# Kernel tuning notes

Measured on AMD Instinct MI355X. Metric: run time of the kernel, lower is better.

The kernel has to match this reference:

```python
import jax, jax.numpy as jnp
import numpy as np

B = 16
NUM_CN = 25000
NUM_VN = 50000
NUM_EDGES = 200000
D_EMBED = 16
D_HIDDEN = 32
D_MSG = 16


def setup_inputs() -> dict:
    key = jax.random.key(0)
    ks = jax.random.split(key, 16)
    def w(k, fan_in, fan_out):
        return jax.random.normal(k, (fan_in, fan_out), dtype=jnp.float32) / jnp.sqrt(jnp.float32(fan_in))
    return {
        "h_from_x": jax.random.normal(ks[0], (B, NUM_CN, D_EMBED), dtype=jnp.float32),
        "h_from_z": jax.random.normal(ks[1], (B, NUM_CN, D_EMBED), dtype=jnp.float32),
        "h_to": jax.random.normal(ks[2], (B, NUM_VN, D_EMBED), dtype=jnp.float32),
        "syndrome_x": jax.random.randint(ks[3], (B, NUM_CN), 0, 2, dtype=jnp.int32),
        "syndrome_z": jax.random.randint(ks[4], (B, NUM_CN), 0, 2, dtype=jnp.int32),
        "from_ind_x": jax.random.randint(ks[5], (NUM_EDGES,), 0, NUM_CN, dtype=jnp.int32),
        "to_ind_x": jax.random.randint(ks[6], (NUM_EDGES,), 0, NUM_VN, dtype=jnp.int32),
        "from_ind_z": jax.random.randint(ks[7], (NUM_EDGES,), 0, NUM_CN, dtype=jnp.int32),
        "to_ind_z": jax.random.randint(ks[8], (NUM_EDGES,), 0, NUM_VN, dtype=jnp.int32),
        # msg MLP x: [2*D_EMBED -> D_HIDDEN (relu) -> D_MSG], no bias
        "Wx1": w(ks[9], 2 * D_EMBED, D_HIDDEN),
        "Wx2": w(ks[10], D_HIDDEN, D_MSG),
        "Wz1": w(ks[11], 2 * D_EMBED, D_HIDDEN),
        "Wz2": w(ks[12], D_HIDDEN, D_MSG),
        # embed MLP: [2*D_MSG + D_EMBED -> D_HIDDEN (relu) -> D_EMBED], no bias
        "We1": w(ks[13], 2 * D_MSG + D_EMBED, D_HIDDEN),
        "We2": w(ks[14], D_HIDDEN, D_EMBED),
    }


def _edge_messages(h_from, h_to, syn, from_ind, to_ind, W1, W2):
    # gather edge endpoint embeddings -> [B, E, 2*D_EMBED]
    feat = jnp.concatenate([h_from[:, from_ind, :], h_to[:, to_ind, :]], axis=-1)
    msg = jnp.maximum(feat @ W1, 0.0) @ W2          # [B, E, D_MSG]
    mask = syn[:, from_ind].astype(msg.dtype)[..., None]
    return msg * mask


def _segment_reduce_sum(msg, to_ind, num_vn):
    # ragged gather+sum per receiving vertex == segment_sum over to_ind
    # msg: [B, E, D] -> [E, B, D] -> segment_sum -> [N, B, D] -> [B, N, D]
    m = jax.ops.segment_sum(jnp.transpose(msg, (1, 0, 2)), to_ind, num_segments=num_vn)
    return jnp.transpose(m, (1, 0, 2))


def reference(h_from_x, h_from_z, h_to, syndrome_x, syndrome_z,
              from_ind_x, to_ind_x, from_ind_z, to_ind_z,
              Wx1, Wx2, Wz1, Wz2, We1, We2):
    num_vn = h_to.shape[1]
    msg_x = _edge_messages(h_from_x, h_to, syndrome_x, from_ind_x, to_ind_x, Wx1, Wx2)
    msg_z = _edge_messages(h_from_z, h_to, syndrome_z, from_ind_z, to_ind_z, Wz1, Wz2)
    m_x = _segment_reduce_sum(msg_x, to_ind_x, num_vn)  # [B, N, D_MSG]
    m_z = _segment_reduce_sum(msg_z, to_ind_z, num_vn)
    feat = jnp.concatenate([m_x, m_z, h_to], axis=-1)   # [B, N, 2*D_MSG+D_EMBED]
    h_to_new = jnp.maximum(feat @ We1, 0.0) @ We2
    return h_to_new
```

## Files before the change

### kernel.cpp

```cpp
#include <hip/hip_runtime.h>

#define NUM_CN   25000
#define NUM_VN   50000
#define NUM_E    200000
#define D_EMBED  16
#define D_HIDDEN 32
#define D_MSG    16
#define BATCH    16

typedef float f32x2 __attribute__((ext_vector_type(2)));

#define WS_IDS_X   0
#define WS_IDS_Z   200000
#define WS_OFF_X   400000
#define WS_OFF_Z   450001
#define WS_CNT_X   500002
#define WS_CNT_Z   550002
#define WS_CUR_X   600002
#define WS_CUR_Z   650002
#define WS_INCL_X  700002
#define WS_INCL_Z  751202
#define WS_PSUM    802402
#define WS_A1X     802816
#define WS_A1Z     7202816
#define SCAN_CHUNKS 49

__device__ __forceinline__ unsigned pack_bf16(float a, float b) {
    unsigned ua = __float_as_uint(a); ua += 0x7fff + ((ua >> 16) & 1);
    unsigned ub = __float_as_uint(b); ub += 0x7fff + ((ub >> 16) & 1);
    return (ua >> 16) | (ub & 0xffff0000u);
}

__global__ __launch_bounds__(256) void hist_a1_kernel(
    const int* __restrict__ ti_x, const int* __restrict__ ti_z,
    const float* __restrict__ h_from_x, const float* __restrict__ h_from_z,
    const int* __restrict__ syn_x, const int* __restrict__ syn_z,
    const float* __restrict__ Wx1, const float* __restrict__ Wz1,
    int* __restrict__ cnt_x, int* __restrict__ cnt_z,
    uint4* __restrict__ a1x, uint4* __restrict__ a1z)
{
    const int t = blockIdx.x * 256 + threadIdx.x;
    if (blockIdx.y == 0) {
        if (t < NUM_E) {
            atomicAdd(&cnt_x[ti_x[t]], 1);
            atomicAdd(&cnt_z[ti_z[t]], 1);
        }
        return;
    }
    if (t >= NUM_CN * BATCH) return;
    const int ch = blockIdx.y - 1;
    const int b  = t & 15;
    const int cn = t >> 4;
    const float* hsrc = (ch ? h_from_z : h_from_x) + ((size_t)b * NUM_CN + cn) * D_EMBED;
    const float* W1   = ch ? Wz1 : Wx1;
    const bool on = ((ch ? syn_z : syn_x)[b * NUM_CN + cn] & 1) != 0;
    uint4* dst = (ch ? a1z : a1x) + (size_t)cn * 64;

    float hf[D_EMBED];
#pragma unroll
    for (int i = 0; i < 4; ++i) {
        float4 v = ((const float4*)hsrc)[i];
        hf[4 * i + 0] = v.x; hf[4 * i + 1] = v.y;
        hf[4 * i + 2] = v.z; hf[4 * i + 3] = v.w;
    }
    f32x2 a[16] = {};
#pragma unroll
    for (int i = 0; i < D_EMBED; ++i) {
        const float fi = hf[i];
        const f32x2* wv = (const f32x2*)(W1 + i * D_HIDDEN);
#pragma unroll
        for (int j = 0; j < 16; ++j)
            a[j] = fi * wv[j] + a[j];
    }
    unsigned u[16];
#pragma unroll
    for (int j = 0; j < 16; ++j)
        u[j] = on ? pack_bf16(a[j].x, a[j].y) : 0xFF80FF80u;
#pragma unroll
    for (int p = 0; p < 4; ++p) {
        uint4 q;
        q.x = u[4 * p + 0]; q.y = u[4 * p + 1];
        q.z = u[4 * p + 2]; q.w = u[4 * p + 3];
        dst[p * 16 + b] = q;
    }
}

__global__ __launch_bounds__(1024) void scan1_kernel(
    const int* __restrict__ cnt_x, const int* __restrict__ cnt_z,
    int* __restrict__ incl_x, int* __restrict__ incl_z,
    int* __restrict__ psum)
{
    __shared__ int s[1024];
    const int ch  = blockIdx.y;
    const int blk = blockIdx.x;
    const int t   = threadIdx.x;
    const int gid = blk * 1024 + t;
    const int* cnt  = ch ? cnt_z  : cnt_x;
    int*       incl = ch ? incl_z : incl_x;
    int v = (gid < NUM_VN) ? cnt[gid] : 0;
    s[t] = v;
    __syncthreads();
#pragma unroll
    for (int d = 1; d < 1024; d <<= 1) {
        int x = 0;
        if (t >= d) x = s[t - d];
        __syncthreads();
        if (t >= d) s[t] += x;
        __syncthreads();
    }
    incl[gid] = s[t];
    if (t == 1023) psum[ch * 64 + blk] = s[1023];
}

__global__ __launch_bounds__(1024) void scan3_kernel(
    const int* __restrict__ cnt_x, const int* __restrict__ cnt_z,
    const int* __restrict__ incl_x, const int* __restrict__ incl_z,
    const int* __restrict__ psum,
    int* __restrict__ off_x, int* __restrict__ off_z,
    int* __restrict__ cur_x, int* __restrict__ cur_z)
{
    const int ch  = blockIdx.y;
    const int blk = blockIdx.x;
    const int t   = threadIdx.x;
    __shared__ int sbase;
    if (t == 0) {
        int run = 0;
        for (int i = 0; i < blk; ++i) run += psum[ch * 64 + i];
        sbase = run;
    }
    __syncthreads();
    const int i = blk * 1024 + t;
    if (i >= NUM_VN) return;
    const int* cnt  = ch ? cnt_z  : cnt_x;
    const int* incl = ch ? incl_z : incl_x;
    int*       off  = ch ? off_z  : off_x;
    int*       cur  = ch ? cur_z  : cur_x;
    int bs = sbase;
    int iv = incl[i];
    off[i + 1] = bs + iv;
    cur[i]     = bs + iv - cnt[i];
    if (i == 0) off[0] = 0;
}

__global__ __launch_bounds__(256) void fill_kernel(
    const int* __restrict__ ti_x, const int* __restrict__ ti_z,
    const int* __restrict__ fi_x, const int* __restrict__ fi_z,
    int* __restrict__ cur_x, int* __restrict__ cur_z,
    int* __restrict__ ids_x, int* __restrict__ ids_z)
{
    int e = blockIdx.x * 256 + threadIdx.x;
    if (e >= NUM_E) return;
    int px = atomicAdd(&cur_x[ti_x[e]], 1);
    ids_x[px] = fi_x[e];
    int pz = atomicAdd(&cur_z[ti_z[e]], 1);
    ids_z[pz] = fi_z[e];
}

__device__ __forceinline__ void acc4(
    unsigned w0, unsigned w1, unsigned w2, unsigned w3,
    const f32x2* __restrict__ a2, f32x2* __restrict__ hacc)
{
    const f32x2 z2 = {0.0f, 0.0f};
    unsigned ww[4] = {w0, w1, w2, w3};
#pragma unroll
    for (int j = 0; j < 4; ++j) {
        f32x2 v;
        v.x = __uint_as_float(ww[j] << 16);
        v.y = __uint_as_float(ww[j] & 0xffff0000u);
        f32x2 s = a2[j] + v;
        s = __builtin_elementwise_max(s, z2);
        hacc[j] += s;
    }
}

__device__ __forceinline__ void channel_accum_store(
    const float* __restrict__ h_to_slot, int n, int b,
    const int* __restrict__ off, const int* __restrict__ ids,
    const uint4* __restrict__ a1,
    const float* __restrict__ W1, const float* __restrict__ W2,
    uint4* __restrict__ dst2)
{
    float ht[D_EMBED];
#pragma unroll
    for (int i = 0; i < 4; ++i) {
        float4 v = ((const float4*)h_to_slot)[i];
        ht[4 * i + 0] = v.x; ht[4 * i + 1] = v.y;
        ht[4 * i + 2] = v.z; ht[4 * i + 3] = v.w;
    }
    f32x2 a2[16] = {};
#pragma unroll
    for (int i = 0; i < D_EMBED; ++i) {
        const float hi = ht[i];
        const f32x2* wv = (const f32x2*)(W1 + (D_EMBED + i) * D_HIDDEN);
#pragma unroll
        for (int p = 0; p < 16; ++p)
            a2[p] = hi * wv[p] + a2[p];
    }

    f32x2 hacc[16] = {};

    const int ks = off[n], ke = off[n + 1];
    for (int k = ks; k < ke; ++k) {
        const uint4* pa = a1 + (size_t)ids[k] * 64 + b;
        uint4 q0 = pa[0], q1 = pa[16], q2 = pa[32], q3 = pa[48];
        acc4(q0.x, q0.y, q0.z, q0.w, a2 + 0,  hacc + 0);
        acc4(q1.x, q1.y, q1.z, q1.w, a2 + 4,  hacc + 4);
        acc4(q2.x, q2.y, q2.z, q2.w, a2 + 8,  hacc + 8);
        acc4(q3.x, q3.y, q3.z, q3.w, a2 + 12, hacc + 12);
    }

    f32x2 m2[8] = {};
#pragma unroll
    for (int p = 0; p < 16; ++p) {
        const float h0 = hacc[p].x, h1 = hacc[p].y;
        const f32x2* w0 = (const f32x2*)(W2 + (2 * p) * D_MSG);
        const f32x2* w1 = (const f32x2*)(W2 + (2 * p + 1) * D_MSG);
#pragma unroll
        for (int j = 0; j < 8; ++j)
            m2[j] = h0 * w0[j] + (h1 * w1[j] + m2[j]);
    }
    uint4 q;
    q.x = pack_bf16(m2[0].x, m2[0].y); q.y = pack_bf16(m2[1].x, m2[1].y);
    q.z = pack_bf16(m2[2].x, m2[2].y); q.w = pack_bf16(m2[3].x, m2[3].y);
    dst2[0] = q;
    q.x = pack_bf16(m2[4].x, m2[4].y); q.y = pack_bf16(m2[5].x, m2[5].y);
    q.z = pack_bf16(m2[6].x, m2[6].y); q.w = pack_bf16(m2[7].x, m2[7].y);
    dst2[1] = q;
}

__global__ __launch_bounds__(256) void gather_kernel(
    const float* __restrict__ h_to,
    const int* __restrict__ off_x, const int* __restrict__ ids_x,
    const int* __restrict__ off_z, const int* __restrict__ ids_z,
    const uint4* __restrict__ a1x, const uint4* __restrict__ a1z,
    const float* __restrict__ Wx1, const float* __restrict__ Wx2,
    const float* __restrict__ Wz1, const float* __restrict__ Wz2,
    uint4* __restrict__ out_m)
{
    const int t = blockIdx.x * 256 + threadIdx.x;
    if (t >= NUM_VN * BATCH) return;
    const int b = t & (BATCH - 1);
    const int n = t >> 4;
    const size_t slot = (size_t)b * NUM_VN + n;
    const float* ht_slot = h_to + slot * D_EMBED;
    uint4* dst = out_m + slot * 4;

    channel_accum_store(ht_slot, n, b, off_x, ids_x, a1x, Wx1, Wx2, dst);
    channel_accum_store(ht_slot, n, b, off_z, ids_z, a1z, Wz1, Wz2, dst + 2);
}

__global__ __launch_bounds__(256) void node_kernel(
    const float* __restrict__ h_to,
    const float* __restrict__ We1, const float* __restrict__ We2,
    float* out)
{
    const f32x2 z2 = {0.0f, 0.0f};
    const int t = blockIdx.x * 256 + threadIdx.x;
    if (t >= NUM_VN * BATCH) return;
    const int b = t & (BATCH - 1);
    const int n = t >> 4;
    const size_t slot = (size_t)b * NUM_VN + n;

    const uint4* pm = (const uint4*)out + slot * 4;
    uint4 q0 = pm[0], q1 = pm[1], q2 = pm[2], q3 = pm[3];
    unsigned uu[16] = {q0.x, q0.y, q0.z, q0.w,
                       q1.x, q1.y, q1.z, q1.w,
                       q2.x, q2.y, q2.z, q2.w,
                       q3.x, q3.y, q3.z, q3.w};
    float f[48];
#pragma unroll
    for (int p = 0; p < 16; ++p) {
        f[2 * p]     = __uint_as_float(uu[p] << 16);
        f[2 * p + 1] = __uint_as_float(uu[p] & 0xffff0000u);
    }
#pragma unroll
    for (int i = 0; i < 4; ++i) {
        float4 v = ((const float4*)(h_to + slot * D_EMBED))[i];
        f[32 + 4 * i + 0] = v.x; f[32 + 4 * i + 1] = v.y;
        f[32 + 4 * i + 2] = v.z; f[32 + 4 * i + 3] = v.w;
    }

    f32x2 hid[16] = {};
#pragma unroll
    for (int i = 0; i < 48; ++i) {
        const float fi = f[i];
        const f32x2* wv = (const f32x2*)(We1 + i * D_HIDDEN);
#pragma unroll
        for (int p = 0; p < 16; ++p)
            hid[p] = fi * wv[p] + hid[p];
    }
#pragma unroll
    for (int p = 0; p < 16; ++p)
        hid[p] = __builtin_elementwise_max(hid[p], z2);

    f32x2 o2[8] = {};
#pragma unroll
    for (int p = 0; p < 16; ++p) {
        const float h0 = hid[p].x, h1 = hid[p].y;
        const f32x2* w0 = (const f32x2*)(We2 + (2 * p) * D_EMBED);
        const f32x2* w1 = (const f32x2*)(We2 + (2 * p + 1) * D_EMBED);
#pragma unroll
        for (int j = 0; j < 8; ++j)
            o2[j] = h0 * w0[j] + (h1 * w1[j] + o2[j]);
    }

#pragma unroll
    for (int i = 0; i < 4; ++i) {
        float4 v;
        v.x = o2[2 * i].x;     v.y = o2[2 * i].y;
        v.z = o2[2 * i + 1].x; v.w = o2[2 * i + 1].y;
        ((float4*)(out + slot * D_EMBED))[i] = v;
    }
}

extern "C" void kernel_launch(void* const* d_in, const int* in_sizes, int n_in,
                              void* d_out, int out_size, void* d_ws, size_t ws_size,
                              hipStream_t stream) {
    const float* h_from_x = (const float*)d_in[0];
    const float* h_from_z = (const float*)d_in[1];
    const float* h_to     = (const float*)d_in[2];
    const int*   syn_x    = (const int*)d_in[3];
    const int*   syn_z    = (const int*)d_in[4];
    const int*   fi_x     = (const int*)d_in[5];
    const int*   ti_x     = (const int*)d_in[6];
    const int*   fi_z     = (const int*)d_in[7];
    const int*   ti_z     = (const int*)d_in[8];
    const float* Wx1      = (const float*)d_in[9];
    const float* Wx2      = (const float*)d_in[10];
    const float* Wz1      = (const float*)d_in[11];
    const float* Wz2      = (const float*)d_in[12];
    const float* We1      = (const float*)d_in[13];
    const float* We2      = (const float*)d_in[14];

    int* ws = (int*)d_ws;
    int* ids_x  = ws + WS_IDS_X;
    int* ids_z  = ws + WS_IDS_Z;
    int* off_x  = ws + WS_OFF_X;
    int* off_z  = ws + WS_OFF_Z;
    int* cnt_x  = ws + WS_CNT_X;
    int* cnt_z  = ws + WS_CNT_Z;
    int* cur_x  = ws + WS_CUR_X;
    int* cur_z  = ws + WS_CUR_Z;
    int* incl_x = ws + WS_INCL_X;
    int* incl_z = ws + WS_INCL_Z;
    int* psum   = ws + WS_PSUM;
    uint4* a1x  = (uint4*)(ws + WS_A1X);
    uint4* a1z  = (uint4*)(ws + WS_A1Z);

    hipMemsetAsync(cnt_x, 0, 2 * NUM_VN * sizeof(int), stream);

    hist_a1_kernel<<<dim3((NUM_CN * BATCH + 255) / 256, 3), dim3(256), 0, stream>>>(
        ti_x, ti_z, h_from_x, h_from_z, syn_x, syn_z, Wx1, Wz1,
        cnt_x, cnt_z, a1x, a1z);
    scan1_kernel<<<dim3(SCAN_CHUNKS, 2), dim3(1024), 0, stream>>>(
        cnt_x, cnt_z, incl_x, incl_z, psum);
    scan3_kernel<<<dim3(SCAN_CHUNKS, 2), dim3(1024), 0, stream>>>(
        cnt_x, cnt_z, incl_x, incl_z, psum, off_x, off_z, cur_x, cur_z);
    fill_kernel<<<dim3((NUM_E + 255) / 256), dim3(256), 0, stream>>>(
        ti_x, ti_z, fi_x, fi_z, cur_x, cur_z, ids_x, ids_z);

    gather_kernel<<<dim3((NUM_VN * BATCH) / 256), dim3(256), 0, stream>>>(
        h_to, off_x, ids_x, off_z, ids_z, a1x, a1z,
        Wx1, Wx2, Wz1, Wz2, (uint4*)d_out);

    node_kernel<<<dim3((NUM_VN * BATCH) / 256), dim3(256), 0, stream>>>(
        h_to, We1, We2, (float*)d_out);
}
```

Measured before the change: 361.1 us.

## Fuse two-pass scan into single-pass decoupled look-back scan

Replaces the two scan kernels (block-local scan plus a separate base-offset pass) with one kernel that uses dynamic block ordering and a decoupled look-back over per-block status words. The status words are zeroed inside the histogram kernel. This removes one kernel launch and the intermediate inclusive-sum buffer traffic. In exchange it adds spin-waiting on global atomics between blocks, and it relies on the launch order given by the atomic ticket to guarantee forward progress.

```diff
diff --git a/kernel.cpp b/kernel.cpp
--- a/kernel.cpp
+++ b/kernel.cpp
@@ -18,9 +18,7 @@
 #define WS_CNT_Z   550002
 #define WS_CUR_X   600002
 #define WS_CUR_Z   650002
-#define WS_INCL_X  700002
-#define WS_INCL_Z  751202
-#define WS_PSUM    802402
+#define WS_STAT    802402
 #define WS_A1X     802816
 #define WS_A1Z     7202816
 #define SCAN_CHUNKS 49
@@ -37,10 +35,12 @@
     const int* __restrict__ syn_x, const int* __restrict__ syn_z,
     const float* __restrict__ Wx1, const float* __restrict__ Wz1,
     int* __restrict__ cnt_x, int* __restrict__ cnt_z,
+    unsigned* __restrict__ stat,
     uint4* __restrict__ a1x, uint4* __restrict__ a1z)
 {
     const int t = blockIdx.x * 256 + threadIdx.x;
     if (blockIdx.y == 0) {
+        if (t < 132) stat[t] = 0;
         if (t < NUM_E) {
             atomicAdd(&cnt_x[ti_x[t]], 1);
             atomicAdd(&cnt_z[ti_z[t]], 1);
@@ -85,20 +85,26 @@
     }
 }
 
-__global__ __launch_bounds__(1024) void scan1_kernel(
+__global__ __launch_bounds__(1024) void scan_kernel(
     const int* __restrict__ cnt_x, const int* __restrict__ cnt_z,
-    int* __restrict__ incl_x, int* __restrict__ incl_z,
-    int* __restrict__ psum)
-{
+    unsigned* __restrict__ stat,
+    int* __restrict__ off_x, int* __restrict__ off_z,
+    int* __restrict__ cur_x, int* __restrict__ cur_z)
+{
+    const int ch = blockIdx.y;
+    const int t  = threadIdx.x;
     __shared__ int s[1024];
-    const int ch  = blockIdx.y;
-    const int blk = blockIdx.x;
-    const int t   = threadIdx.x;
-    const int gid = blk * 1024 + t;
-    const int* cnt  = ch ? cnt_z  : cnt_x;
-    int*       incl = ch ? incl_z : incl_x;
-    int v = (gid < NUM_VN) ? cnt[gid] : 0;
-    s[t] = v;
+    __shared__ int vb_sh, base_sh;
+    unsigned* st = stat + ch * 64;
+    if (t == 0) vb_sh = (int)atomicAdd(&stat[128 + ch], 1u);
+    __syncthreads();
+    const int vb  = vb_sh;
+    const int gid = vb * 1024 + t;
+    const int* cnt = ch ? cnt_z : cnt_x;
+    int* off = ch ? off_z : off_x;
+    int* cur = ch ? cur_z : cur_x;
+    const int c = (gid < NUM_VN) ? cnt[gid] : 0;
+    s[t] = c;
     __syncthreads();
 #pragma unroll
     for (int d = 1; d < 1024; d <<= 1) {
@@ -108,38 +114,28 @@
         if (t >= d) s[t] += x;
         __syncthreads();
     }
-    incl[gid] = s[t];
-    if (t == 1023) psum[ch * 64 + blk] = s[1023];
-}
-
-__global__ __launch_bounds__(1024) void scan3_kernel(
-    const int* __restrict__ cnt_x, const int* __restrict__ cnt_z,
-    const int* __restrict__ incl_x, const int* __restrict__ incl_z,
-    const int* __restrict__ psum,
-    int* __restrict__ off_x, int* __restrict__ off_z,
-    int* __restrict__ cur_x, int* __restrict__ cur_z)
-{
-    const int ch  = blockIdx.y;
-    const int blk = blockIdx.x;
-    const int t   = threadIdx.x;
-    __shared__ int sbase;
+    if (t == 1023) atomicExch(&st[vb], (1u << 30) | (unsigned)s[1023]);
     if (t == 0) {
-        int run = 0;
-        for (int i = 0; i < blk; ++i) run += psum[ch * 64 + i];
-        sbase = run;
+        int base = 0;
+        for (int j = vb - 1; j >= 0; ) {
+            unsigned v = atomicOr(&st[j], 0u);
+            if (v == 0u) continue;
+            base += (int)(v & 0x3fffffffu);
+            if (v & 0x80000000u) break;
+            --j;
+        }
+        base_sh = base;
     }
     __syncthreads();
-    const int i = blk * 1024 + t;
-    if (i >= NUM_VN) return;
-    const int* cnt  = ch ? cnt_z  : cnt_x;
-    const int* incl = ch ? incl_z : incl_x;
-    int*       off  = ch ? off_z  : off_x;
-    int*       cur  = ch ? cur_z  : cur_x;
-    int bs = sbase;
-    int iv = incl[i];
-    off[i + 1] = bs + iv;
-    cur[i]     = bs + iv - cnt[i];
-    if (i == 0) off[0] = 0;
+    const int base = base_sh;
+    if (t == 1023)
+        atomicExch(&st[vb], 0x80000000u | (unsigned)(base + s[1023]));
+    if (gid < NUM_VN) {
+        int iv = base + s[t];
+        off[gid + 1] = iv;
+        cur[gid]     = iv - c;
+    }
+    if (vb == 0 && t == 0) off[0] = 0;
 }
 
 __global__ __launch_bounds__(256) void fill_kernel(
@@ -341,9 +337,7 @@
     int* cnt_z  = ws + WS_CNT_Z;
     int* cur_x  = ws + WS_CUR_X;
     int* cur_z  = ws + WS_CUR_Z;
-    int* incl_x = ws + WS_INCL_X;
-    int* incl_z = ws + WS_INCL_Z;
-    int* psum   = ws + WS_PSUM;
+    unsigned* stat = (unsigned*)(ws + WS_STAT);
     uint4* a1x  = (uint4*)(ws + WS_A1X);
     uint4* a1z  = (uint4*)(ws + WS_A1Z);
 
@@ -351,11 +345,9 @@
 
     hist_a1_kernel<<<dim3((NUM_CN * BATCH + 255) / 256, 3), dim3(256), 0, stream>>>(
         ti_x, ti_z, h_from_x, h_from_z, syn_x, syn_z, Wx1, Wz1,
-        cnt_x, cnt_z, a1x, a1z);
-    scan1_kernel<<<dim3(SCAN_CHUNKS, 2), dim3(1024), 0, stream>>>(
-        cnt_x, cnt_z, incl_x, incl_z, psum);
-    scan3_kernel<<<dim3(SCAN_CHUNKS, 2), dim3(1024), 0, stream>>>(
-        cnt_x, cnt_z, incl_x, incl_z, psum, off_x, off_z, cur_x, cur_z);
+        cnt_x, cnt_z, stat, a1x, a1z);
+    scan_kernel<<<dim3(SCAN_CHUNKS, 2), dim3(1024), 0, stream>>>(
+        cnt_x, cnt_z, stat, off_x, off_z, cur_x, cur_z);
     fill_kernel<<<dim3((NUM_E + 255) / 256), dim3(256), 0, stream>>>(
         ti_x, ti_z, fi_x, fi_z, cur_x, cur_z, ids_x, ids_z);
 
```

After: 362.2 us. About the same (+0.3%).
